# Kernel optimization log

Measured on AMD Instinct MI355X. Metric: run time of the kernel, lower is better.

Reference implementation:

```python
import jax, jax.numpy as jnp
import numpy as np

DIM_V = 1024
NUM_HEADS = 64            # per the module arg name; actually the per-chunk size
DIM_SPLIT = DIM_V // NUM_HEADS  # 16 = effective number of attention heads (module quirk)
N_Q, N_K = 2048, 2048
DIM_Q, DIM_K = 1024, 1024


def setup_inputs() -> dict:
    key = jax.random.key(0)
    ks = jax.random.split(key, 10)
    s = 0.02
    return {
        "Q": jax.random.normal(ks[0], (N_Q, DIM_Q), dtype=jnp.float32),
        "K": jax.random.normal(ks[1], (N_K, DIM_K), dtype=jnp.float32),
        "Wq": jax.random.normal(ks[2], (DIM_V, DIM_Q), dtype=jnp.float32) * s,
        "bq": jax.random.normal(ks[3], (DIM_V,), dtype=jnp.float32) * s,
        "Wk": jax.random.normal(ks[4], (DIM_V, DIM_K), dtype=jnp.float32) * s,
        "bk": jax.random.normal(ks[5], (DIM_V,), dtype=jnp.float32) * s,
        "Wv": jax.random.normal(ks[6], (DIM_V, DIM_K), dtype=jnp.float32) * s,
        "bv": jax.random.normal(ks[7], (DIM_V,), dtype=jnp.float32) * s,
        "Wo": jax.random.normal(ks[8], (DIM_V, DIM_V), dtype=jnp.float32) * s,
        "bo": jax.random.normal(ks[9], (DIM_V,), dtype=jnp.float32) * s,
    }


def _split_heads(x):
    # jnp.split(x[None], DIM_SPLIT, axis=2) then concat on axis 0 ==
    # [DIM_SPLIT, n, NUM_HEADS] with chunk h = x[:, h*NUM_HEADS:(h+1)*NUM_HEADS]
    n = x.shape[0]
    return x.reshape(n, DIM_SPLIT, NUM_HEADS).transpose(1, 0, 2)


def reference(Q, K, Wq, bq, Wk, bk, Wv, bv, Wo, bo):
    q = Q @ Wq.T + bq            # [n_q, dim_V]
    k = K @ Wk.T + bk            # [n_k, dim_V]
    v = K @ Wv.T + bv            # [n_k, dim_V]
    Q_ = _split_heads(q)         # [H, n_q, d] with H=DIM_SPLIT, d=NUM_HEADS
    K_ = _split_heads(k)
    V_ = _split_heads(v)
    # Faithful to source: softmax first, THEN divide by sqrt(dim_V)
    A = jax.nn.softmax(jnp.einsum('hqd,hkd->hqk', Q_, K_), axis=-1)
    A = A / jnp.sqrt(jnp.float32(DIM_V))
    O = (Q_ + jnp.einsum('hqk,hkd->hqd', A, V_)).reshape(-1, DIM_V)  # [n_q, dim_V]
    # res1 = identity (ln=False)
    O = O + jax.nn.relu(O @ Wo.T + bo)
    # res2 = identity (ln=False)
    return O
```

## Files before the change

### kernel.cpp

```cpp
#include <hip/hip_runtime.h>
#include <hip/hip_bf16.h>
#include <cstdint>

typedef unsigned short u16;
typedef __attribute__((ext_vector_type(8))) short short8;
typedef __attribute__((ext_vector_type(4))) float f32x4;

__device__ __forceinline__ u16 f2b(float f) {
  uint32_t u = __float_as_uint(f);
  u += 0x7fffu + ((u >> 16) & 1u);
  return (u16)(u >> 16);
}
__device__ __forceinline__ float b2f(u16 b) {
  return __uint_as_float(((uint32_t)b) << 16);
}
__device__ __forceinline__ uint32_t pk2bf(float a, float b) {
  __hip_bfloat162 t = __float22bfloat162_rn(make_float2(a, b));
  return *(uint32_t*)&t;
}

__global__ __launch_bounds__(256) void cast_all(
    const float* __restrict__ Q, const float* __restrict__ K,
    const float* __restrict__ Wq, const float* __restrict__ Wk,
    const float* __restrict__ Wv, const float* __restrict__ Wo,
    u16* __restrict__ xq, u16* __restrict__ xk,
    u16* __restrict__ wq, u16* __restrict__ wk,
    u16* __restrict__ wv, u16* __restrict__ wo) {
  int g = blockIdx.x * 256 + threadIdx.x;
  const float* src; u16* dst; int off;
  if      (g <  524288) { src = Q;  dst = xq; off = g; }
  else if (g < 1048576) { src = K;  dst = xk; off = g -  524288; }
  else if (g < 1310720) { src = Wq; dst = wq; off = g - 1048576; }
  else if (g < 1572864) { src = Wk; dst = wk; off = g - 1310720; }
  else if (g < 1835008) { src = Wv; dst = wv; off = g - 1572864; }
  else                  { src = Wo; dst = wo; off = g - 1835008; }
  float4 v = reinterpret_cast<const float4*>(src)[off];
  ushort4 o4;
  o4.x = f2b(v.x); o4.y = f2b(v.y); o4.z = f2b(v.z); o4.w = f2b(v.w);
  reinterpret_cast<ushort4*>(dst)[off] = o4;
}

__global__ __launch_bounds__(256) void gemm3(
    const u16* __restrict__ xq, const u16* __restrict__ xk,
    const u16* __restrict__ wq, const u16* __restrict__ wk,
    const u16* __restrict__ wv,
    const float* __restrict__ bq, const float* __restrict__ bk,
    const float* __restrict__ bv,
    u16* __restrict__ qb, u16* __restrict__ kb, u16* __restrict__ vT) {
  __shared__ __align__(16) u16 sA[64 * 72];
  __shared__ __align__(16) u16 sB[64 * 72];
  const int t = threadIdx.x, blk = blockIdx.x, z = blockIdx.y;
  const int xcd = blk & 7, lid = blk >> 3;
  const u16 *A, *B; const float* bias; u16* C; int ldC, mbase, nbase; bool brow;
  if (z == 0)      { A = xq; B = wq; bias = bq; C = qb; ldC = 1024;
                     mbase = (xcd * 4 + (lid >> 4)) * 64; nbase = (lid & 15) * 64; brow = false; }
  else if (z == 1) { A = xk; B = wk; bias = bk; C = kb; ldC = 1024;
                     mbase = (xcd * 4 + (lid >> 4)) * 64; nbase = (lid & 15) * 64; brow = false; }
  else             { A = wv; B = xk; bias = bv; C = vT; ldC = 2048;
                     mbase = (xcd * 2 + (lid >> 5)) * 64; nbase = (lid & 31) * 64; brow = true; }
  const int lane = t & 63, wid = t >> 6;
  const int wy = wid >> 1, wx = wid & 1;
  const int m = lane & 15, quad = lane >> 4;
  const int srow = t >> 2, scb = (t & 3) * 16;
  const u16* gA = A + (mbase + srow) * 1024 + scb;
  const u16* gB = B + (nbase + srow) * 1024 + scb;
  uint4 ra0 = *(const uint4*)(gA), ra1 = *(const uint4*)(gA + 8);
  uint4 rb0 = *(const uint4*)(gB), rb1 = *(const uint4*)(gB + 8);

  f32x4 acc[2][2];
#pragma unroll
  for (int i = 0; i < 2; i++)
#pragma unroll
    for (int j = 0; j < 2; j++) acc[i][j] = (f32x4){0.f, 0.f, 0.f, 0.f};

  for (int kb_ = 0; kb_ < 16; ++kb_) {
    __syncthreads();
    *(uint4*)(&sA[srow * 72 + scb])     = ra0;
    *(uint4*)(&sA[srow * 72 + scb + 8]) = ra1;
    *(uint4*)(&sB[srow * 72 + scb])     = rb0;
    *(uint4*)(&sB[srow * 72 + scb + 8]) = rb1;
    if (kb_ < 15) {
      ra0 = *(const uint4*)(gA + (kb_ + 1) * 64);
      ra1 = *(const uint4*)(gA + (kb_ + 1) * 64 + 8);
      rb0 = *(const uint4*)(gB + (kb_ + 1) * 64);
      rb1 = *(const uint4*)(gB + (kb_ + 1) * 64 + 8);
    }
    __syncthreads();
    short8 af[2][2], bf[2][2];
#pragma unroll
    for (int mi = 0; mi < 2; mi++)
#pragma unroll
      for (int ks = 0; ks < 2; ks++)
        af[mi][ks] = *(const short8*)(
            &sA[(wy * 32 + mi * 16 + m) * 72 + ks * 32 + quad * 8]);
#pragma unroll
    for (int ni = 0; ni < 2; ni++)
#pragma unroll
      for (int ks = 0; ks < 2; ks++)
        bf[ni][ks] = *(const short8*)(
            &sB[(wx * 32 + ni * 16 + m) * 72 + ks * 32 + quad * 8]);
#pragma unroll
    for (int ks = 0; ks < 2; ks++)
#pragma unroll
      for (int mi = 0; mi < 2; mi++)
#pragma unroll
        for (int ni = 0; ni < 2; ni++)
          acc[mi][ni] = __builtin_amdgcn_mfma_f32_16x16x32_bf16(
              af[mi][ks], bf[ni][ks], acc[mi][ni], 0, 0, 0);
  }

#pragma unroll
  for (int mi = 0; mi < 2; mi++)
#pragma unroll
    for (int ni = 0; ni < 2; ni++) {
      const int col = nbase + wx * 32 + ni * 16 + m;
      const float bcol = brow ? 0.f : bias[col];
#pragma unroll
      for (int r = 0; r < 4; r++) {
        const int row = mbase + wy * 32 + mi * 16 + quad * 4 + r;
        const float bval = brow ? bias[row] : bcol;
        C[row * ldC + col] = f2b(acc[mi][ni][r] + bval);
      }
    }
}

__global__ __launch_bounds__(256) void gemm_out(
    const u16* __restrict__ A, const u16* __restrict__ B,
    const float* __restrict__ bias, const u16* __restrict__ Res,
    float* __restrict__ out) {
  __shared__ __align__(16) u16 sA[64 * 72];
  __shared__ __align__(16) u16 sB[64 * 72];
  const int t = threadIdx.x, blk = blockIdx.x;
  const int xcd = blk & 7, lid = blk >> 3;
  const int mbase = (xcd * 4 + (lid >> 4)) * 64, nbase = (lid & 15) * 64;
  const int lane = t & 63, wid = t >> 6;
  const int wy = wid >> 1, wx = wid & 1;
  const int m = lane & 15, quad = lane >> 4;
  const int srow = t >> 2, scb = (t & 3) * 16;
  const u16* gA = A + (mbase + srow) * 1024 + scb;
  const u16* gB = B + (nbase + srow) * 1024 + scb;
  uint4 ra0 = *(const uint4*)(gA), ra1 = *(const uint4*)(gA + 8);
  uint4 rb0 = *(const uint4*)(gB), rb1 = *(const uint4*)(gB + 8);

  f32x4 acc[2][2];
#pragma unroll
  for (int i = 0; i < 2; i++)
#pragma unroll
    for (int j = 0; j < 2; j++) acc[i][j] = (f32x4){0.f, 0.f, 0.f, 0.f};

  for (int kb_ = 0; kb_ < 16; ++kb_) {
    __syncthreads();
    *(uint4*)(&sA[srow * 72 + scb])     = ra0;
    *(uint4*)(&sA[srow * 72 + scb + 8]) = ra1;
    *(uint4*)(&sB[srow * 72 + scb])     = rb0;
    *(uint4*)(&sB[srow * 72 + scb + 8]) = rb1;
    if (kb_ < 15) {
      ra0 = *(const uint4*)(gA + (kb_ + 1) * 64);
      ra1 = *(const uint4*)(gA + (kb_ + 1) * 64 + 8);
      rb0 = *(const uint4*)(gB + (kb_ + 1) * 64);
      rb1 = *(const uint4*)(gB + (kb_ + 1) * 64 + 8);
    }
    __syncthreads();
    short8 af[2][2], bf[2][2];
#pragma unroll
    for (int mi = 0; mi < 2; mi++)
#pragma unroll
      for (int ks = 0; ks < 2; ks++)
        af[mi][ks] = *(const short8*)(
            &sA[(wy * 32 + mi * 16 + m) * 72 + ks * 32 + quad * 8]);
#pragma unroll
    for (int ni = 0; ni < 2; ni++)
#pragma unroll
      for (int ks = 0; ks < 2; ks++)
        bf[ni][ks] = *(const short8*)(
            &sB[(wx * 32 + ni * 16 + m) * 72 + ks * 32 + quad * 8]);
#pragma unroll
    for (int ks = 0; ks < 2; ks++)
#pragma unroll
      for (int mi = 0; mi < 2; mi++)
#pragma unroll
        for (int ni = 0; ni < 2; ni++)
          acc[mi][ni] = __builtin_amdgcn_mfma_f32_16x16x32_bf16(
              af[mi][ks], bf[ni][ks], acc[mi][ni], 0, 0, 0);
  }

#pragma unroll
  for (int mi = 0; mi < 2; mi++)
#pragma unroll
    for (int ni = 0; ni < 2; ni++) {
      const int col = nbase + wx * 32 + ni * 16 + m;
      const float bcol = bias[col];
#pragma unroll
      for (int r = 0; r < 4; r++) {
        const int row = mbase + wy * 32 + mi * 16 + quad * 4 + r;
        out[row * 1024 + col] =
            b2f(Res[row * 1024 + col]) + fmaxf(acc[mi][ni][r] + bcol, 0.f);
      }
    }
}

__global__ __launch_bounds__(256, 2) void flash(
    const u16* __restrict__ q, const u16* __restrict__ k,
    const u16* __restrict__ vT, u16* __restrict__ po, float* __restrict__ lp) {
  __shared__ __align__(16) u16 sK[64 * 72];
  __shared__ __align__(16) u16 sV[64 * 72];
  __shared__ __align__(16) u16 sP[4 * 64 * 72];
  const int t = threadIdx.x;
  const int qt = blockIdx.x, h = blockIdx.y, sp = blockIdx.z;
  const int lane = t & 63, wid = t >> 6;
  const int m = lane & 15, quad = lane >> 4;
  const int colbase = h * 64;
  const int pbase = wid * 4608;
  const int kbase = sp * 512;
  const int qwave = qt * 256 + wid * 64;

  short8 aq[4][2];
#pragma unroll
  for (int mi = 0; mi < 4; mi++)
#pragma unroll
    for (int g = 0; g < 2; g++)
      aq[mi][g] = *(const short8*)(
          &q[(qwave + mi * 16 + m) * 1024 + colbase + g * 32 + quad * 8]);

  f32x4 o[4][4];
  float lpart[4] = {0.f, 0.f, 0.f, 0.f};
#pragma unroll
  for (int mi = 0; mi < 4; mi++)
#pragma unroll
    for (int nt = 0; nt < 4; nt++) o[mi][nt] = (f32x4){0.f, 0.f, 0.f, 0.f};

  const int srow = t >> 2, scb = (t & 3) * 16;
  const u16* gK = k + (kbase + srow) * 1024 + colbase + scb;
  const u16* gV = vT + (colbase + srow) * 2048 + kbase + scb;

  uint4 rk0 = *(const uint4*)(gK), rk1 = *(const uint4*)(gK + 8);
  uint4 rv0 = *(const uint4*)(gV), rv1 = *(const uint4*)(gV + 8);

  uint32_t* sP32 = (uint32_t*)sP;

  for (int kt = 0; kt < 8; ++kt) {
    __syncthreads();
    *(uint4*)(&sK[srow * 72 + scb])     = rk0;
    *(uint4*)(&sK[srow * 72 + scb + 8]) = rk1;
    *(uint4*)(&sV[srow * 72 + scb])     = rv0;
    *(uint4*)(&sV[srow * 72 + scb + 8]) = rv1;
    if (kt < 7) {
      rk0 = *(const uint4*)(gK + (kt + 1) * 65536);
      rk1 = *(const uint4*)(gK + (kt + 1) * 65536 + 8);
      rv0 = *(const uint4*)(gV + (kt + 1) * 64);
      rv1 = *(const uint4*)(gV + (kt + 1) * 64 + 8);
    }
    __syncthreads();

#pragma unroll
    for (int nt = 0; nt < 4; nt++) {
      short8 bk0 = *(const short8*)(&sK[(nt * 16 + m) * 72 + quad * 8]);
      short8 bk1 = *(const short8*)(&sK[(nt * 16 + m) * 72 + 32 + quad * 8]);
#pragma unroll
      for (int mi = 0; mi < 4; mi++) {
        f32x4 st = (f32x4){0.f, 0.f, 0.f, 0.f};
        st = __builtin_amdgcn_mfma_f32_16x16x32_bf16(bk0, aq[mi][0], st, 0, 0, 0);
        st = __builtin_amdgcn_mfma_f32_16x16x32_bf16(bk1, aq[mi][1], st, 0, 0, 0);
        float p0 = __expf(st[0] - 16.0f);
        float p1 = __expf(st[1] - 16.0f);
        float p2 = __expf(st[2] - 16.0f);
        float p3 = __expf(st[3] - 16.0f);
        lpart[mi] += (p0 + p1) + (p2 + p3);
        const int pa_ = pbase + (mi * 16 + m) * 72 + nt * 16 + quad * 4;
        sP32[pa_ >> 1]       = pk2bf(p0, p1);
        sP32[(pa_ >> 1) + 1] = pk2bf(p2, p3);
      }
    }

    short8 pa[4][2];
#pragma unroll
    for (int mi = 0; mi < 4; mi++)
#pragma unroll
      for (int g = 0; g < 2; g++)
        pa[mi][g] = *(const short8*)(&sP[pbase + (mi * 16 + m) * 72 + g * 32 + quad * 8]);
#pragma unroll
    for (int nt = 0; nt < 4; nt++) {
      short8 bv0 = *(const short8*)(&sV[(nt * 16 + m) * 72 + quad * 8]);
      short8 bv1 = *(const short8*)(&sV[(nt * 16 + m) * 72 + 32 + quad * 8]);
#pragma unroll
      for (int mi = 0; mi < 4; mi++) {
        o[mi][nt] = __builtin_amdgcn_mfma_f32_16x16x32_bf16(pa[mi][0], bv0, o[mi][nt], 0, 0, 0);
        o[mi][nt] = __builtin_amdgcn_mfma_f32_16x16x32_bf16(pa[mi][1], bv1, o[mi][nt], 0, 0, 0);
      }
    }
  }

#pragma unroll
  for (int mi = 0; mi < 4; mi++) {
    float l = lpart[mi];
    l += __shfl_xor(l, 16);
    l += __shfl_xor(l, 32);
    if (quad == 0)
      lp[(sp * 16 + h) * 2048 + qwave + mi * 16 + m] = l;
  }

  u16* sO = &sP[pbase];
#pragma unroll
  for (int mi = 0; mi < 4; mi++)
#pragma unroll
    for (int nt = 0; nt < 4; nt++)
#pragma unroll
      for (int r = 0; r < 4; r++)
        sO[(mi * 16 + quad * 4 + r) * 72 + nt * 16 + m] = f2b(o[mi][nt][r]);

  const int rrow = lane >> 3, rcol = (lane & 7) * 8;
  const int gbase = ((sp * 16 + h) * 2048 + qwave) * 64;
#pragma unroll
  for (int g = 0; g < 8; g++) {
    const int row = g * 8 + rrow;
    short8 v = *(const short8*)&sO[row * 72 + rcol];
    *(short8*)&po[gbase + row * 64 + rcol] = v;
  }
}

__global__ __launch_bounds__(256) void combine(
    const u16* __restrict__ po, const float* __restrict__ lp,
    const u16* __restrict__ qb, u16* __restrict__ ob) {
  const int idx = blockIdx.x * 256 + threadIdx.x;
  const int dq = idx & 15, qg = (idx >> 4) & 2047, h = idx >> 15;
  float acc0 = 0.f, acc1 = 0.f, acc2 = 0.f, acc3 = 0.f, l = 0.f;
#pragma unroll
  for (int s = 0; s < 4; s++) {
    const ushort4 p4 = *(const ushort4*)&po[(((s * 16 + h) * 2048 + qg) * 64) + dq * 4];
    acc0 += b2f(p4.x); acc1 += b2f(p4.y); acc2 += b2f(p4.z); acc3 += b2f(p4.w);
    l += lp[(s * 16 + h) * 2048 + qg];
  }
  const float inv = 1.0f / (l * 32.0f);
  const ushort4 q4 = *(const ushort4*)&qb[qg * 1024 + h * 64 + dq * 4];
  ushort4 o4;
  o4.x = f2b(b2f(q4.x) + acc0 * inv);
  o4.y = f2b(b2f(q4.y) + acc1 * inv);
  o4.z = f2b(b2f(q4.z) + acc2 * inv);
  o4.w = f2b(b2f(q4.w) + acc3 * inv);
  *(ushort4*)&ob[(h * 128 + (qg >> 4)) * 1024 + (qg & 15) * 64 + dq * 4] = o4;
}

extern "C" void kernel_launch(void* const* d_in, const int* in_sizes, int n_in,
                              void* d_out, int out_size, void* d_ws, size_t ws_size,
                              hipStream_t stream) {
  const float* Q  = (const float*)d_in[0];
  const float* K  = (const float*)d_in[1];
  const float* Wq = (const float*)d_in[2];
  const float* bq = (const float*)d_in[3];
  const float* Wk = (const float*)d_in[4];
  const float* bk = (const float*)d_in[5];
  const float* Wv = (const float*)d_in[6];
  const float* bv = (const float*)d_in[7];
  const float* Wo = (const float*)d_in[8];
  const float* bo = (const float*)d_in[9];
  float* out = (float*)d_out;

  u16* ws = (u16*)d_ws;
  u16* xq  = ws;
  u16* xk  = xq  + 2097152;
  u16* wqb = xk  + 2097152;
  u16* wkb = wqb + 1048576;
  u16* wvb = wkb + 1048576;
  u16* wob = wvb + 1048576;
  u16* qb  = wob + 1048576;
  u16* kb  = qb  + 2097152;
  u16* vT  = kb  + 2097152;
  u16* ob  = vT  + 2097152;
  u16* po  = ob  + 2097152;
  float* lp = (float*)(po + 8388608);

  cast_all<<<8192, 256, 0, stream>>>(Q, K, Wq, Wk, Wv, Wo, xq, xk, wqb, wkb, wvb, wob);

  gemm3<<<dim3(512, 3), 256, 0, stream>>>(xq, xk, wqb, wkb, wvb, bq, bk, bv, qb, kb, vT);

  flash<<<dim3(8, 16, 4), 256, 0, stream>>>(qb, kb, vT, po, lp);

  combine<<<2048, 256, 0, stream>>>(po, lp, qb, ob);

  gemm_out<<<512, 256, 0, stream>>>(ob, wob, bo, ob, out);
}
```

Before: 163.4 us.

## Fuse fp32-to-bf16 casts into GEMM loads and split-K combine into flash

Removes the separate cast kernel: the GEMMs now load fp32 inputs and weights directly and convert to bf16 while staging into shared memory. Also drops the combine kernel: each flash block increments an atomic counter per (head, q-tile), and the last of the four split blocks reduces the partial outputs and writes the combined result. This saves two launches and the round trip of the bf16 copies through memory. In exchange, the GEMMs read twice the bytes per tile, a memset is added, and the tail block serialises the combine work with threadfence ordering.

```diff
diff --git a/kernel.cpp b/kernel.cpp
--- a/kernel.cpp
+++ b/kernel.cpp
@@ -18,32 +18,17 @@
   __hip_bfloat162 t = __float22bfloat162_rn(make_float2(a, b));
   return *(uint32_t*)&t;
 }
-
-__global__ __launch_bounds__(256) void cast_all(
+__device__ __forceinline__ uint4 pk8(const float4 a, const float4 b) {
+  uint4 r;
+  r.x = pk2bf(a.x, a.y); r.y = pk2bf(a.z, a.w);
+  r.z = pk2bf(b.x, b.y); r.w = pk2bf(b.z, b.w);
+  return r;
+}
+
+__global__ __launch_bounds__(256) void gemm3(
     const float* __restrict__ Q, const float* __restrict__ K,
     const float* __restrict__ Wq, const float* __restrict__ Wk,
-    const float* __restrict__ Wv, const float* __restrict__ Wo,
-    u16* __restrict__ xq, u16* __restrict__ xk,
-    u16* __restrict__ wq, u16* __restrict__ wk,
-    u16* __restrict__ wv, u16* __restrict__ wo) {
-  int g = blockIdx.x * 256 + threadIdx.x;
-  const float* src; u16* dst; int off;
-  if      (g <  524288) { src = Q;  dst = xq; off = g; }
-  else if (g < 1048576) { src = K;  dst = xk; off = g -  524288; }
-  else if (g < 1310720) { src = Wq; dst = wq; off = g - 1048576; }
-  else if (g < 1572864) { src = Wk; dst = wk; off = g - 1310720; }
-  else if (g < 1835008) { src = Wv; dst = wv; off = g - 1572864; }
-  else                  { src = Wo; dst = wo; off = g - 1835008; }
-  float4 v = reinterpret_cast<const float4*>(src)[off];
-  ushort4 o4;
-  o4.x = f2b(v.x); o4.y = f2b(v.y); o4.z = f2b(v.z); o4.w = f2b(v.w);
-  reinterpret_cast<ushort4*>(dst)[off] = o4;
-}
-
-__global__ __launch_bounds__(256) void gemm3(
-    const u16* __restrict__ xq, const u16* __restrict__ xk,
-    const u16* __restrict__ wq, const u16* __restrict__ wk,
-    const u16* __restrict__ wv,
+    const float* __restrict__ Wv,
     const float* __restrict__ bq, const float* __restrict__ bk,
     const float* __restrict__ bv,
     u16* __restrict__ qb, u16* __restrict__ kb, u16* __restrict__ vT) {
@@ -51,21 +36,23 @@
   __shared__ __align__(16) u16 sB[64 * 72];
   const int t = threadIdx.x, blk = blockIdx.x, z = blockIdx.y;
   const int xcd = blk & 7, lid = blk >> 3;
-  const u16 *A, *B; const float* bias; u16* C; int ldC, mbase, nbase; bool brow;
-  if (z == 0)      { A = xq; B = wq; bias = bq; C = qb; ldC = 1024;
+  const float *A, *B; const float* bias; u16* C; int ldC, mbase, nbase; bool brow;
+  if (z == 0)      { A = Q;  B = Wq; bias = bq; C = qb; ldC = 1024;
                      mbase = (xcd * 4 + (lid >> 4)) * 64; nbase = (lid & 15) * 64; brow = false; }
-  else if (z == 1) { A = xk; B = wk; bias = bk; C = kb; ldC = 1024;
+  else if (z == 1) { A = K;  B = Wk; bias = bk; C = kb; ldC = 1024;
                      mbase = (xcd * 4 + (lid >> 4)) * 64; nbase = (lid & 15) * 64; brow = false; }
-  else             { A = wv; B = xk; bias = bv; C = vT; ldC = 2048;
+  else             { A = Wv; B = K;  bias = bv; C = vT; ldC = 2048;
                      mbase = (xcd * 2 + (lid >> 5)) * 64; nbase = (lid & 31) * 64; brow = true; }
   const int lane = t & 63, wid = t >> 6;
   const int wy = wid >> 1, wx = wid & 1;
   const int m = lane & 15, quad = lane >> 4;
   const int srow = t >> 2, scb = (t & 3) * 16;
-  const u16* gA = A + (mbase + srow) * 1024 + scb;
-  const u16* gB = B + (nbase + srow) * 1024 + scb;
-  uint4 ra0 = *(const uint4*)(gA), ra1 = *(const uint4*)(gA + 8);
-  uint4 rb0 = *(const uint4*)(gB), rb1 = *(const uint4*)(gB + 8);
+  const float* gA = A + (mbase + srow) * 1024 + scb;
+  const float* gB = B + (nbase + srow) * 1024 + scb;
+  float4 ra0 = *(const float4*)(gA),     ra1 = *(const float4*)(gA + 4);
+  float4 ra2 = *(const float4*)(gA + 8), ra3 = *(const float4*)(gA + 12);
+  float4 rb0 = *(const float4*)(gB),     rb1 = *(const float4*)(gB + 4);
+  float4 rb2 = *(const float4*)(gB + 8), rb3 = *(const float4*)(gB + 12);
 
   f32x4 acc[2][2];
 #pragma unroll
@@ -75,15 +62,17 @@
 
   for (int kb_ = 0; kb_ < 16; ++kb_) {
     __syncthreads();
-    *(uint4*)(&sA[srow * 72 + scb])     = ra0;
-    *(uint4*)(&sA[srow * 72 + scb + 8]) = ra1;
-    *(uint4*)(&sB[srow * 72 + scb])     = rb0;
-    *(uint4*)(&sB[srow * 72 + scb + 8]) = rb1;
+    *(uint4*)(&sA[srow * 72 + scb])     = pk8(ra0, ra1);
+    *(uint4*)(&sA[srow * 72 + scb + 8]) = pk8(ra2, ra3);
+    *(uint4*)(&sB[srow * 72 + scb])     = pk8(rb0, rb1);
+    *(uint4*)(&sB[srow * 72 + scb + 8]) = pk8(rb2, rb3);
     if (kb_ < 15) {
-      ra0 = *(const uint4*)(gA + (kb_ + 1) * 64);
-      ra1 = *(const uint4*)(gA + (kb_ + 1) * 64 + 8);
-      rb0 = *(const uint4*)(gB + (kb_ + 1) * 64);
-      rb1 = *(const uint4*)(gB + (kb_ + 1) * 64 + 8);
+      const float* pA = gA + (kb_ + 1) * 64;
+      ra0 = *(const float4*)(pA);     ra1 = *(const float4*)(pA + 4);
+      ra2 = *(const float4*)(pA + 8); ra3 = *(const float4*)(pA + 12);
+      const float* pB = gB + (kb_ + 1) * 64;
+      rb0 = *(const float4*)(pB);     rb1 = *(const float4*)(pB + 4);
+      rb2 = *(const float4*)(pB + 8); rb3 = *(const float4*)(pB + 12);
     }
     __syncthreads();
     short8 af[2][2], bf[2][2];
@@ -124,8 +113,158 @@
     }
 }
 
+__global__ __launch_bounds__(256, 2) void flash(
+    const u16* __restrict__ q, const u16* __restrict__ k,
+    const u16* __restrict__ vT, u16* __restrict__ po, float* __restrict__ lp,
+    u16* __restrict__ ob, unsigned* __restrict__ cnt) {
+  __shared__ __align__(16) u16 sK[64 * 72];
+  __shared__ __align__(16) u16 sV[64 * 72];
+  __shared__ __align__(16) u16 sP[4 * 64 * 72];
+  __shared__ unsigned s_old;
+  const int t = threadIdx.x;
+  const int qt = blockIdx.x, h = blockIdx.y, sp = blockIdx.z;
+  const int lane = t & 63, wid = t >> 6;
+  const int m = lane & 15, quad = lane >> 4;
+  const int colbase = h * 64;
+  const int pbase = wid * 4608;
+  const int kbase = sp * 512;
+  const int qwave = qt * 256 + wid * 64;
+
+  short8 aq[4][2];
+#pragma unroll
+  for (int mi = 0; mi < 4; mi++)
+#pragma unroll
+    for (int g = 0; g < 2; g++)
+      aq[mi][g] = *(const short8*)(
+          &q[(qwave + mi * 16 + m) * 1024 + colbase + g * 32 + quad * 8]);
+
+  f32x4 o[4][4];
+  float lpart[4] = {0.f, 0.f, 0.f, 0.f};
+#pragma unroll
+  for (int mi = 0; mi < 4; mi++)
+#pragma unroll
+    for (int nt = 0; nt < 4; nt++) o[mi][nt] = (f32x4){0.f, 0.f, 0.f, 0.f};
+
+  const int srow = t >> 2, scb = (t & 3) * 16;
+  const u16* gK = k + (kbase + srow) * 1024 + colbase + scb;
+  const u16* gV = vT + (colbase + srow) * 2048 + kbase + scb;
+
+  uint4 rk0 = *(const uint4*)(gK), rk1 = *(const uint4*)(gK + 8);
+  uint4 rv0 = *(const uint4*)(gV), rv1 = *(const uint4*)(gV + 8);
+
+  uint32_t* sP32 = (uint32_t*)sP;
+
+  for (int kt = 0; kt < 8; ++kt) {
+    __syncthreads();
+    *(uint4*)(&sK[srow * 72 + scb])     = rk0;
+    *(uint4*)(&sK[srow * 72 + scb + 8]) = rk1;
+    *(uint4*)(&sV[srow * 72 + scb])     = rv0;
+    *(uint4*)(&sV[srow * 72 + scb + 8]) = rv1;
+    if (kt < 7) {
+      rk0 = *(const uint4*)(gK + (kt + 1) * 65536);
+      rk1 = *(const uint4*)(gK + (kt + 1) * 65536 + 8);
+      rv0 = *(const uint4*)(gV + (kt + 1) * 64);
+      rv1 = *(const uint4*)(gV + (kt + 1) * 64 + 8);
+    }
+    __syncthreads();
+
+#pragma unroll
+    for (int nt = 0; nt < 4; nt++) {
+      short8 bk0 = *(const short8*)(&sK[(nt * 16 + m) * 72 + quad * 8]);
+      short8 bk1 = *(const short8*)(&sK[(nt * 16 + m) * 72 + 32 + quad * 8]);
+#pragma unroll
+      for (int mi = 0; mi < 4; mi++) {
+        f32x4 st = (f32x4){0.f, 0.f, 0.f, 0.f};
+        st = __builtin_amdgcn_mfma_f32_16x16x32_bf16(bk0, aq[mi][0], st, 0, 0, 0);
+        st = __builtin_amdgcn_mfma_f32_16x16x32_bf16(bk1, aq[mi][1], st, 0, 0, 0);
+        float p0 = __expf(st[0] - 16.0f);
+        float p1 = __expf(st[1] - 16.0f);
+        float p2 = __expf(st[2] - 16.0f);
+        float p3 = __expf(st[3] - 16.0f);
+        lpart[mi] += (p0 + p1) + (p2 + p3);
+        const int pa_ = pbase + (mi * 16 + m) * 72 + nt * 16 + quad * 4;
+        sP32[pa_ >> 1]       = pk2bf(p0, p1);
+        sP32[(pa_ >> 1) + 1] = pk2bf(p2, p3);
+      }
+    }
+
+    short8 pa[4][2];
+#pragma unroll
+    for (int mi = 0; mi < 4; mi++)
+#pragma unroll
+      for (int g = 0; g < 2; g++)
+        pa[mi][g] = *(const short8*)(&sP[pbase + (mi * 16 + m) * 72 + g * 32 + quad * 8]);
+#pragma unroll
+    for (int nt = 0; nt < 4; nt++) {
+      short8 bv0 = *(const short8*)(&sV[(nt * 16 + m) * 72 + quad * 8]);
+      short8 bv1 = *(const short8*)(&sV[(nt * 16 + m) * 72 + 32 + quad * 8]);
+#pragma unroll
+      for (int mi = 0; mi < 4; mi++) {
+        o[mi][nt] = __builtin_amdgcn_mfma_f32_16x16x32_bf16(pa[mi][0], bv0, o[mi][nt], 0, 0, 0);
+        o[mi][nt] = __builtin_amdgcn_mfma_f32_16x16x32_bf16(pa[mi][1], bv1, o[mi][nt], 0, 0, 0);
+      }
+    }
+  }
+
+#pragma unroll
+  for (int mi = 0; mi < 4; mi++) {
+    float l = lpart[mi];
+    l += __shfl_xor(l, 16);
+    l += __shfl_xor(l, 32);
+    if (quad == 0)
+      lp[(sp * 16 + h) * 2048 + qwave + mi * 16 + m] = l;
+  }
+
+  u16* sO = &sP[pbase];
+#pragma unroll
+  for (int mi = 0; mi < 4; mi++)
+#pragma unroll
+    for (int nt = 0; nt < 4; nt++)
+#pragma unroll
+      for (int r = 0; r < 4; r++)
+        sO[(mi * 16 + quad * 4 + r) * 72 + nt * 16 + m] = f2b(o[mi][nt][r]);
+
+  const int rrow = lane >> 3, rcol = (lane & 7) * 8;
+  const int gbase = ((sp * 16 + h) * 2048 + qwave) * 64;
+#pragma unroll
+  for (int g = 0; g < 8; g++) {
+    const int row = g * 8 + rrow;
+    short8 v = *(const short8*)&sO[row * 72 + rcol];
+    *(short8*)&po[gbase + row * 64 + rcol] = v;
+  }
+
+  __threadfence();
+  __syncthreads();
+  if (t == 0) s_old = atomicAdd(&cnt[h * 8 + qt], 1u);
+  __syncthreads();
+  if (s_old == 3u) {
+    __threadfence();
+#pragma unroll
+    for (int i = 0; i < 16; ++i) {
+      const int il = i * 256 + t;
+      const int dq = il & 15, qgl = il >> 4;
+      const int qg = qt * 256 + qgl;
+      float acc0 = 0.f, acc1 = 0.f, acc2 = 0.f, acc3 = 0.f, l = 0.f;
+#pragma unroll
+      for (int s = 0; s < 4; s++) {
+        const ushort4 p4 = *(const ushort4*)&po[(((s * 16 + h) * 2048 + qg) * 64) + dq * 4];
+        acc0 += b2f(p4.x); acc1 += b2f(p4.y); acc2 += b2f(p4.z); acc3 += b2f(p4.w);
+        l += lp[(s * 16 + h) * 2048 + qg];
+      }
+      const float inv = 1.0f / (l * 32.0f);
+      const ushort4 q4 = *(const ushort4*)&q[qg * 1024 + h * 64 + dq * 4];
+      ushort4 o4;
+      o4.x = f2b(b2f(q4.x) + acc0 * inv);
+      o4.y = f2b(b2f(q4.y) + acc1 * inv);
+      o4.z = f2b(b2f(q4.z) + acc2 * inv);
+      o4.w = f2b(b2f(q4.w) + acc3 * inv);
+      *(ushort4*)&ob[(h * 128 + (qg >> 4)) * 1024 + (qg & 15) * 64 + dq * 4] = o4;
+    }
+  }
+}
+
 __global__ __launch_bounds__(256) void gemm_out(
-    const u16* __restrict__ A, const u16* __restrict__ B,
+    const u16* __restrict__ A, const float* __restrict__ B,
     const float* __restrict__ bias, const u16* __restrict__ Res,
     float* __restrict__ out) {
   __shared__ __align__(16) u16 sA[64 * 72];
@@ -138,9 +277,10 @@
   const int m = lane & 15, quad = lane >> 4;
   const int srow = t >> 2, scb = (t & 3) * 16;
   const u16* gA = A + (mbase + srow) * 1024 + scb;
-  const u16* gB = B + (nbase + srow) * 1024 + scb;
+  const float* gB = B + (nbase + srow) * 1024 + scb;
   uint4 ra0 = *(const uint4*)(gA), ra1 = *(const uint4*)(gA + 8);
-  uint4 rb0 = *(const uint4*)(gB), rb1 = *(const uint4*)(gB + 8);
+  float4 rb0 = *(const float4*)(gB),     rb1 = *(const float4*)(gB + 4);
+  float4 rb2 = *(const float4*)(gB + 8), rb3 = *(const float4*)(gB + 12);
 
   f32x4 acc[2][2];
 #pragma unroll
@@ -152,13 +292,14 @@
     __syncthreads();
     *(uint4*)(&sA[srow * 72 + scb])     = ra0;
     *(uint4*)(&sA[srow * 72 + scb + 8]) = ra1;
-    *(uint4*)(&sB[srow * 72 + scb])     = rb0;
-    *(uint4*)(&sB[srow * 72 + scb + 8]) = rb1;
+    *(uint4*)(&sB[srow * 72 + scb])     = pk8(rb0, rb1);
+    *(uint4*)(&sB[srow * 72 + scb + 8]) = pk8(rb2, rb3);
     if (kb_ < 15) {
       ra0 = *(const uint4*)(gA + (kb_ + 1) * 64);
       ra1 = *(const uint4*)(gA + (kb_ + 1) * 64 + 8);
-      rb0 = *(const uint4*)(gB + (kb_ + 1) * 64);
-      rb1 = *(const uint4*)(gB + (kb_ + 1) * 64 + 8);
+      const float* pB = gB + (kb_ + 1) * 64;
+      rb0 = *(const float4*)(pB);     rb1 = *(const float4*)(pB + 4);
+      rb2 = *(const float4*)(pB + 8); rb3 = *(const float4*)(pB + 12);
     }
     __syncthreads();
     short8 af[2][2], bf[2][2];
@@ -197,147 +338,6 @@
             b2f(Res[row * 1024 + col]) + fmaxf(acc[mi][ni][r] + bcol, 0.f);
       }
     }
-}
-
-__global__ __launch_bounds__(256, 2) void flash(
-    const u16* __restrict__ q, const u16* __restrict__ k,
-    const u16* __restrict__ vT, u16* __restrict__ po, float* __restrict__ lp) {
-  __shared__ __align__(16) u16 sK[64 * 72];
-  __shared__ __align__(16) u16 sV[64 * 72];
-  __shared__ __align__(16) u16 sP[4 * 64 * 72];
-  const int t = threadIdx.x;
-  const int qt = blockIdx.x, h = blockIdx.y, sp = blockIdx.z;
-  const int lane = t & 63, wid = t >> 6;
-  const int m = lane & 15, quad = lane >> 4;
-  const int colbase = h * 64;
-  const int pbase = wid * 4608;
-  const int kbase = sp * 512;
-  const int qwave = qt * 256 + wid * 64;
-
-  short8 aq[4][2];
-#pragma unroll
-  for (int mi = 0; mi < 4; mi++)
-#pragma unroll
-    for (int g = 0; g < 2; g++)
-      aq[mi][g] = *(const short8*)(
-          &q[(qwave + mi * 16 + m) * 1024 + colbase + g * 32 + quad * 8]);
-
-  f32x4 o[4][4];
-  float lpart[4] = {0.f, 0.f, 0.f, 0.f};
-#pragma unroll
-  for (int mi = 0; mi < 4; mi++)
-#pragma unroll
-    for (int nt = 0; nt < 4; nt++) o[mi][nt] = (f32x4){0.f, 0.f, 0.f, 0.f};
-
-  const int srow = t >> 2, scb = (t & 3) * 16;
-  const u16* gK = k + (kbase + srow) * 1024 + colbase + scb;
-  const u16* gV = vT + (colbase + srow) * 2048 + kbase + scb;
-
-  uint4 rk0 = *(const uint4*)(gK), rk1 = *(const uint4*)(gK + 8);
-  uint4 rv0 = *(const uint4*)(gV), rv1 = *(const uint4*)(gV + 8);
-
-  uint32_t* sP32 = (uint32_t*)sP;
-
-  for (int kt = 0; kt < 8; ++kt) {
-    __syncthreads();
-    *(uint4*)(&sK[srow * 72 + scb])     = rk0;
-    *(uint4*)(&sK[srow * 72 + scb + 8]) = rk1;
-    *(uint4*)(&sV[srow * 72 + scb])     = rv0;
-    *(uint4*)(&sV[srow * 72 + scb + 8]) = rv1;
-    if (kt < 7) {
-      rk0 = *(const uint4*)(gK + (kt + 1) * 65536);
-      rk1 = *(const uint4*)(gK + (kt + 1) * 65536 + 8);
-      rv0 = *(const uint4*)(gV + (kt + 1) * 64);
-      rv1 = *(const uint4*)(gV + (kt + 1) * 64 + 8);
-    }
-    __syncthreads();
-
-#pragma unroll
-    for (int nt = 0; nt < 4; nt++) {
-      short8 bk0 = *(const short8*)(&sK[(nt * 16 + m) * 72 + quad * 8]);
-      short8 bk1 = *(const short8*)(&sK[(nt * 16 + m) * 72 + 32 + quad * 8]);
-#pragma unroll
-      for (int mi = 0; mi < 4; mi++) {
-        f32x4 st = (f32x4){0.f, 0.f, 0.f, 0.f};
-        st = __builtin_amdgcn_mfma_f32_16x16x32_bf16(bk0, aq[mi][0], st, 0, 0, 0);
-        st = __builtin_amdgcn_mfma_f32_16x16x32_bf16(bk1, aq[mi][1], st, 0, 0, 0);
-        float p0 = __expf(st[0] - 16.0f);
-        float p1 = __expf(st[1] - 16.0f);
-        float p2 = __expf(st[2] - 16.0f);
-        float p3 = __expf(st[3] - 16.0f);
-        lpart[mi] += (p0 + p1) + (p2 + p3);
-        const int pa_ = pbase + (mi * 16 + m) * 72 + nt * 16 + quad * 4;
-        sP32[pa_ >> 1]       = pk2bf(p0, p1);
-        sP32[(pa_ >> 1) + 1] = pk2bf(p2, p3);
-      }
-    }
-
-    short8 pa[4][2];
-#pragma unroll
-    for (int mi = 0; mi < 4; mi++)
-#pragma unroll
-      for (int g = 0; g < 2; g++)
-        pa[mi][g] = *(const short8*)(&sP[pbase + (mi * 16 + m) * 72 + g * 32 + quad * 8]);
-#pragma unroll
-    for (int nt = 0; nt < 4; nt++) {
-      short8 bv0 = *(const short8*)(&sV[(nt * 16 + m) * 72 + quad * 8]);
-      short8 bv1 = *(const short8*)(&sV[(nt * 16 + m) * 72 + 32 + quad * 8]);
-#pragma unroll
-      for (int mi = 0; mi < 4; mi++) {
-        o[mi][nt] = __builtin_amdgcn_mfma_f32_16x16x32_bf16(pa[mi][0], bv0, o[mi][nt], 0, 0, 0);
-        o[mi][nt] = __builtin_amdgcn_mfma_f32_16x16x32_bf16(pa[mi][1], bv1, o[mi][nt], 0, 0, 0);
-      }
-    }
-  }
-
-#pragma unroll
-  for (int mi = 0; mi < 4; mi++) {
-    float l = lpart[mi];
-    l += __shfl_xor(l, 16);
-    l += __shfl_xor(l, 32);
-    if (quad == 0)
-      lp[(sp * 16 + h) * 2048 + qwave + mi * 16 + m] = l;
-  }
-
-  u16* sO = &sP[pbase];
-#pragma unroll
-  for (int mi = 0; mi < 4; mi++)
-#pragma unroll
-    for (int nt = 0; nt < 4; nt++)
-#pragma unroll
-      for (int r = 0; r < 4; r++)
-        sO[(mi * 16 + quad * 4 + r) * 72 + nt * 16 + m] = f2b(o[mi][nt][r]);
-
-  const int rrow = lane >> 3, rcol = (lane & 7) * 8;
-  const int gbase = ((sp * 16 + h) * 2048 + qwave) * 64;
-#pragma unroll
-  for (int g = 0; g < 8; g++) {
-    const int row = g * 8 + rrow;
-    short8 v = *(const short8*)&sO[row * 72 + rcol];
-    *(short8*)&po[gbase + row * 64 + rcol] = v;
-  }
-}
-
-__global__ __launch_bounds__(256) void combine(
-    const u16* __restrict__ po, const float* __restrict__ lp,
-    const u16* __restrict__ qb, u16* __restrict__ ob) {
-  const int idx = blockIdx.x * 256 + threadIdx.x;
-  const int dq = idx & 15, qg = (idx >> 4) & 2047, h = idx >> 15;
-  float acc0 = 0.f, acc1 = 0.f, acc2 = 0.f, acc3 = 0.f, l = 0.f;
-#pragma unroll
-  for (int s = 0; s < 4; s++) {
-    const ushort4 p4 = *(const ushort4*)&po[(((s * 16 + h) * 2048 + qg) * 64) + dq * 4];
-    acc0 += b2f(p4.x); acc1 += b2f(p4.y); acc2 += b2f(p4.z); acc3 += b2f(p4.w);
-    l += lp[(s * 16 + h) * 2048 + qg];
-  }
-  const float inv = 1.0f / (l * 32.0f);
-  const ushort4 q4 = *(const ushort4*)&qb[qg * 1024 + h * 64 + dq * 4];
-  ushort4 o4;
-  o4.x = f2b(b2f(q4.x) + acc0 * inv);
-  o4.y = f2b(b2f(q4.y) + acc1 * inv);
-  o4.z = f2b(b2f(q4.z) + acc2 * inv);
-  o4.w = f2b(b2f(q4.w) + acc3 * inv);
-  *(ushort4*)&ob[(h * 128 + (qg >> 4)) * 1024 + (qg & 15) * 64 + dq * 4] = o4;
 }
 
 extern "C" void kernel_launch(void* const* d_in, const int* in_sizes, int n_in,
@@ -356,26 +356,20 @@
   float* out = (float*)d_out;
 
   u16* ws = (u16*)d_ws;
-  u16* xq  = ws;
-  u16* xk  = xq  + 2097152;
-  u16* wqb = xk  + 2097152;
-  u16* wkb = wqb + 1048576;
-  u16* wvb = wkb + 1048576;
-  u16* wob = wvb + 1048576;
-  u16* qb  = wob + 1048576;
+  u16* qb  = ws;
   u16* kb  = qb  + 2097152;
   u16* vT  = kb  + 2097152;
   u16* ob  = vT  + 2097152;
   u16* po  = ob  + 2097152;
   float* lp = (float*)(po + 8388608);
-
-  cast_all<<<8192, 256, 0, stream>>>(Q, K, Wq, Wk, Wv, Wo, xq, xk, wqb, wkb, wvb, wob);
-
-  gemm3<<<dim3(512, 3), 256, 0, stream>>>(xq, xk, wqb, wkb, wvb, bq, bk, bv, qb, kb, vT);
-
-  flash<<<dim3(8, 16, 4), 256, 0, stream>>>(qb, kb, vT, po, lp);
-
-  combine<<<2048, 256, 0, stream>>>(po, lp, qb, ob);
-
-  gemm_out<<<512, 256, 0, stream>>>(ob, wob, bo, ob, out);
-}
+  unsigned* cnt = (unsigned*)(lp + 131072);
+
+  hipMemsetAsync(cnt, 0, 512, stream);
+
+  gemm3<<<dim3(512, 3), 256, 0, stream>>>(Q, K, Wq, Wk, Wv, bq, bk, bv,
+                                          qb, kb, vT);
+
+  flash<<<dim3(8, 16, 4), 256, 0, stream>>>(qb, kb, vT, po, lp, ob, cnt);
+
+  gemm_out<<<512, 256, 0, stream>>>(ob, Wo, bo, ob, out);
+}
```

After: 258.4 us. 1.58x slower.
